# Performance work log

Measured on AMD Instinct MI355X. Metric: run time of the kernel, lower is better.

## Reference

```python
import jax, jax.numpy as jnp
import numpy as np

EPS = 1e-10  # PyTorch Adagrad epsilon convention: denom = sqrt(m) + eps


def setup_inputs() -> dict:
    key = jax.random.key(0)
    k1, k2, k3, k4 = jax.random.split(key, 4)
    N, V, D = 262144, 500000, 64
    return {
        "gradients": jax.random.normal(k1, (N, D), dtype=jnp.float32),
        "weights": jax.random.normal(k2, (V, D), dtype=jnp.float32),
        "moments": jax.random.uniform(k3, (V, D), dtype=jnp.float32),
        "indices": jax.random.randint(k4, (N,), 0, V, dtype=jnp.int64),
        "learning_rate": jnp.ones((), dtype=jnp.float32),
        "valid_count": 200000,  # python int (static)
    }


def reference(gradients, weights, moments, indices, learning_rate, valid_count):
    # Sparse Adagrad: gather rows by index, m += g^2, w -= lr*g/(sqrt(m)+eps), scatter back.
    N = gradients.shape[0]
    valid = (jnp.arange(N) < valid_count)[:, None]          # [N,1] mask of valid rows
    g = jnp.where(valid, gradients, jnp.zeros((), gradients.dtype))  # [N,D]

    # Accumulate squared grads into moments (duplicate indices accumulate).
    moments_new = moments.at[indices].add(g * g)            # [V,D]

    # Per-row denominator uses the fully-accumulated moment of that index.
    denom = jnp.sqrt(moments_new[indices]) + EPS            # [N,D] gather
    weights_new = weights.at[indices].add(-learning_rate * g / denom)  # [V,D]

    return weights_new, moments_new
```

## Files before the change

### kernel.cpp

```cpp
#include <hip/hip_runtime.h>

#define ADAGRAD_EPS 1e-10f

typedef float f4 __attribute__((ext_vector_type(4)));


__global__ void build_lists_kernel(const int* __restrict__ idx,
                                   const int* __restrict__ vc_p,
                                   int* __restrict__ head,
                                   int* __restrict__ next) {
    int vc = *vc_p;
    int r = blockIdx.x * blockDim.x + threadIdx.x;
    if (r >= vc) return;
    int i = idx[r];
    next[r] = atomicExch(&head[i], r);
}

__global__ __launch_bounds__(256) void apply_kernel(
        const f4* __restrict__ g4,
        const f4* __restrict__ w4,
        const f4* __restrict__ m4,
        const int* __restrict__ head,
        const int* __restrict__ next,
        const float* __restrict__ lr_p,
        f4* __restrict__ ow4,
        f4* __restrict__ om4,
        int V) {
    int t = blockIdx.x * blockDim.x + threadIdx.x;
    int v = t >> 3;
    if (v >= V) return;
    int d2 = (t & 7) << 1;
    int off = v * 16 + d2;

    int r = head[v];
    f4 w0 = w4[off];
    f4 w1 = w4[off + 1];
    f4 m0 = m4[off];
    f4 m1 = m4[off + 1];

    if (r < 0) {
        __builtin_nontemporal_store(w0, ow4 + off);
        __builtin_nontemporal_store(w1, ow4 + off + 1);
        __builtin_nontemporal_store(m0, om4 + off);
        __builtin_nontemporal_store(m1, om4 + off + 1);
        return;
    }

    float lr = *lr_p;

    f4 s10 = {0.f, 0.f, 0.f, 0.f};
    f4 s11 = s10, s20 = s10, s21 = s10;
    while (r >= 0) {
        int go = r * 16 + d2;
        f4 g0 = g4[go];
        f4 g1 = g4[go + 1];
        r = next[r];
        s10 += g0; s20 += g0 * g0;
        s11 += g1; s21 += g1 * g1;
    }

    f4 mn0 = m0 + s20;
    f4 mn1 = m1 + s21;
    __builtin_nontemporal_store(mn0, om4 + off);
    __builtin_nontemporal_store(mn1, om4 + off + 1);

    f4 wn0, wn1;
    wn0.x = w0.x - lr * s10.x / (sqrtf(mn0.x) + ADAGRAD_EPS);
    wn0.y = w0.y - lr * s10.y / (sqrtf(mn0.y) + ADAGRAD_EPS);
    wn0.z = w0.z - lr * s10.z / (sqrtf(mn0.z) + ADAGRAD_EPS);
    wn0.w = w0.w - lr * s10.w / (sqrtf(mn0.w) + ADAGRAD_EPS);
    wn1.x = w1.x - lr * s11.x / (sqrtf(mn1.x) + ADAGRAD_EPS);
    wn1.y = w1.y - lr * s11.y / (sqrtf(mn1.y) + ADAGRAD_EPS);
    wn1.z = w1.z - lr * s11.z / (sqrtf(mn1.z) + ADAGRAD_EPS);
    wn1.w = w1.w - lr * s11.w / (sqrtf(mn1.w) + ADAGRAD_EPS);
    __builtin_nontemporal_store(wn0, ow4 + off);
    __builtin_nontemporal_store(wn1, ow4 + off + 1);
}

extern "C" void kernel_launch(void* const* d_in, const int* in_sizes, int n_in,
                              void* d_out, int out_size, void* d_ws, size_t ws_size,
                              hipStream_t stream) {
    const float* g   = (const float*)d_in[0];
    const float* w   = (const float*)d_in[1];
    const float* m   = (const float*)d_in[2];
    const int*   idx = (const int*)d_in[3];
    const float* lr  = (const float*)d_in[4];
    const int*   vc  = (const int*)d_in[5];

    long long ND = in_sizes[0];
    long long VD = in_sizes[1];
    int N = (int)(ND / 64);
    int V = (int)(VD / 64);

    float* out_w = (float*)d_out;
    float* out_m = (float*)d_out + VD;

    int* head = (int*)d_ws;
    int* next = head + V;

    hipMemsetAsync(head, 0xFF, (size_t)V * sizeof(int), stream);

    build_lists_kernel<<<(N + 255) / 256, 256, 0, stream>>>(idx, vc, head, next);

    long long apply_threads = (long long)V * 8;
    apply_kernel<<<(int)((apply_threads + 255) / 256), 256, 0, stream>>>(
        (const f4*)g, (const f4*)w, (const f4*)m,
        head, next, lr, (f4*)out_w, (f4*)out_m, V);
}
```

Measured before the change: 486.0 us.

## Split apply into dense copy and compacted update over touched rows

```diff
diff --git a/kernel.cpp b/kernel.cpp
--- a/kernel.cpp
+++ b/kernel.cpp
@@ -8,27 +8,48 @@
 __global__ void build_lists_kernel(const int* __restrict__ idx,
                                    const int* __restrict__ vc_p,
                                    int* __restrict__ head,
-                                   int* __restrict__ next) {
+                                   int* __restrict__ next,
+                                   int* __restrict__ tlist,
+                                   int* __restrict__ cnt) {
     int vc = *vc_p;
     int r = blockIdx.x * blockDim.x + threadIdx.x;
     if (r >= vc) return;
     int i = idx[r];
-    next[r] = atomicExch(&head[i], r);
+    int prev = atomicExch(&head[i], r);
+    next[r] = prev;
+    if (prev < 0) {
+        int slot = atomicAdd(cnt, 1);
+        tlist[slot] = i;
+    }
 }
 
-__global__ __launch_bounds__(256) void apply_kernel(
+__global__ __launch_bounds__(256) void copy_kernel(
+        const f4* __restrict__ w4,
+        const f4* __restrict__ m4,
+        f4* __restrict__ ow4,
+        f4* __restrict__ om4,
+        int n4) {
+    int i = blockIdx.x * blockDim.x + threadIdx.x;
+    if (i >= n4) return;
+    ow4[i] = w4[i];
+    om4[i] = m4[i];
+}
+
+__global__ __launch_bounds__(256) void update_kernel(
         const f4* __restrict__ g4,
         const f4* __restrict__ w4,
         const f4* __restrict__ m4,
         const int* __restrict__ head,
         const int* __restrict__ next,
+        const int* __restrict__ tlist,
+        const int* __restrict__ cnt,
         const float* __restrict__ lr_p,
         f4* __restrict__ ow4,
-        f4* __restrict__ om4,
-        int V) {
+        f4* __restrict__ om4) {
     int t = blockIdx.x * blockDim.x + threadIdx.x;
-    int v = t >> 3;
-    if (v >= V) return;
+    int s = t >> 3;
+    if (s >= *cnt) return;
+    int v = tlist[s];
     int d2 = (t & 7) << 1;
     int off = v * 16 + d2;
 
@@ -37,15 +58,6 @@
     f4 w1 = w4[off + 1];
     f4 m0 = m4[off];
     f4 m1 = m4[off + 1];
-
-    if (r < 0) {
-        __builtin_nontemporal_store(w0, ow4 + off);
-        __builtin_nontemporal_store(w1, ow4 + off + 1);
-        __builtin_nontemporal_store(m0, om4 + off);
-        __builtin_nontemporal_store(m1, om4 + off + 1);
-        return;
-    }
-
     float lr = *lr_p;
 
     f4 s10 = {0.f, 0.f, 0.f, 0.f};
@@ -61,8 +73,8 @@
 
     f4 mn0 = m0 + s20;
     f4 mn1 = m1 + s21;
-    __builtin_nontemporal_store(mn0, om4 + off);
-    __builtin_nontemporal_store(mn1, om4 + off + 1);
+    om4[off]     = mn0;
+    om4[off + 1] = mn1;
 
     f4 wn0, wn1;
     wn0.x = w0.x - lr * s10.x / (sqrtf(mn0.x) + ADAGRAD_EPS);
@@ -73,8 +85,8 @@
     wn1.y = w1.y - lr * s11.y / (sqrtf(mn1.y) + ADAGRAD_EPS);
     wn1.z = w1.z - lr * s11.z / (sqrtf(mn1.z) + ADAGRAD_EPS);
     wn1.w = w1.w - lr * s11.w / (sqrtf(mn1.w) + ADAGRAD_EPS);
-    __builtin_nontemporal_store(wn0, ow4 + off);
-    __builtin_nontemporal_store(wn1, ow4 + off + 1);
+    ow4[off]     = wn0;
+    ow4[off + 1] = wn1;
 }
 
 extern "C" void kernel_launch(void* const* d_in, const int* in_sizes, int n_in,
@@ -95,15 +107,23 @@
     float* out_w = (float*)d_out;
     float* out_m = (float*)d_out + VD;
 
-    int* head = (int*)d_ws;
-    int* next = head + V;
+    int* head  = (int*)d_ws;
+    int* next  = head + V;
+    int* tlist = next + N;
+    int* cnt   = tlist + N;
 
     hipMemsetAsync(head, 0xFF, (size_t)V * sizeof(int), stream);
+    hipMemsetAsync(cnt, 0, sizeof(int), stream);
 
-    build_lists_kernel<<<(N + 255) / 256, 256, 0, stream>>>(idx, vc, head, next);
+    build_lists_kernel<<<(N + 255) / 256, 256, 0, stream>>>(
+        idx, vc, head, next, tlist, cnt);
 
-    long long apply_threads = (long long)V * 8;
-    apply_kernel<<<(int)((apply_threads + 255) / 256), 256, 0, stream>>>(
+    int n4 = (int)(VD / 4);
+    copy_kernel<<<(n4 + 255) / 256, 256, 0, stream>>>(
+        (const f4*)w, (const f4*)m, (f4*)out_w, (f4*)out_m, n4);
+
+    long long upd_threads = (long long)N * 8;
+    update_kernel<<<(int)((upd_threads + 255) / 256), 256, 0, stream>>>(
         (const f4*)g, (const f4*)w, (const f4*)m,
-        head, next, lr, (f4*)out_w, (f4*)out_m, V);
+        head, next, tlist, cnt, lr, (f4*)out_w, (f4*)out_m);
 }
```

Result: slower. 536.3 us (+10.4%).

## Interleave two row chains per thread with one f4 per lane

Applied to the files above, without the earlier changes.

```diff
diff --git a/kernel.cpp b/kernel.cpp
--- a/kernel.cpp
+++ b/kernel.cpp
@@ -25,56 +25,69 @@
         const float* __restrict__ lr_p,
         f4* __restrict__ ow4,
         f4* __restrict__ om4,
-        int V) {
+        int V, int H) {
     int t = blockIdx.x * blockDim.x + threadIdx.x;
-    int v = t >> 3;
-    if (v >= V) return;
-    int d2 = (t & 7) << 1;
-    int off = v * 16 + d2;
+    int v0 = t >> 4;
+    if (v0 >= H) return;
+    int d = t & 15;
+    int v1 = v0 + H;
+    bool has1 = (v1 < V);
 
-    int r = head[v];
-    f4 w0 = w4[off];
-    f4 w1 = w4[off + 1];
-    f4 m0 = m4[off];
-    f4 m1 = m4[off + 1];
+    int off0 = v0 * 16 + d;
+    int off1 = v1 * 16 + d;
 
-    if (r < 0) {
-        __builtin_nontemporal_store(w0, ow4 + off);
-        __builtin_nontemporal_store(w1, ow4 + off + 1);
-        __builtin_nontemporal_store(m0, om4 + off);
-        __builtin_nontemporal_store(m1, om4 + off + 1);
+    int r0 = head[v0];
+    int r1 = has1 ? head[v1] : -1;
+
+    f4 z = {0.f, 0.f, 0.f, 0.f};
+    f4 w0 = w4[off0];
+    f4 m0 = m4[off0];
+    f4 w1 = has1 ? w4[off1] : z;
+    f4 m1 = has1 ? m4[off1] : z;
+
+    float lr = *lr_p;
+
+    if ((r0 & r1) < 0) {
+        ow4[off0] = w0;
+        om4[off0] = m0;
+        if (has1) { ow4[off1] = w1; om4[off1] = m1; }
         return;
     }
 
-    float lr = *lr_p;
-
-    f4 s10 = {0.f, 0.f, 0.f, 0.f};
-    f4 s11 = s10, s20 = s10, s21 = s10;
-    while (r >= 0) {
-        int go = r * 16 + d2;
-        f4 g0 = g4[go];
-        f4 g1 = g4[go + 1];
-        r = next[r];
-        s10 += g0; s20 += g0 * g0;
-        s11 += g1; s21 += g1 * g1;
+    f4 a1 = z, a2 = z;
+    f4 b1 = z, b2 = z;
+    while (r0 >= 0 || r1 >= 0) {
+        if (r0 >= 0) {
+            f4 g0 = g4[r0 * 16 + d];
+            r0 = next[r0];
+            a1 += g0; a2 += g0 * g0;
+        }
+        if (r1 >= 0) {
+            f4 g1 = g4[r1 * 16 + d];
+            r1 = next[r1];
+            b1 += g1; b2 += g1 * g1;
+        }
     }
 
-    f4 mn0 = m0 + s20;
-    f4 mn1 = m1 + s21;
-    __builtin_nontemporal_store(mn0, om4 + off);
-    __builtin_nontemporal_store(mn1, om4 + off + 1);
+    f4 mn0 = m0 + a2;
+    om4[off0] = mn0;
+    f4 wn0;
+    wn0.x = w0.x - lr * a1.x / (sqrtf(mn0.x) + ADAGRAD_EPS);
+    wn0.y = w0.y - lr * a1.y / (sqrtf(mn0.y) + ADAGRAD_EPS);
+    wn0.z = w0.z - lr * a1.z / (sqrtf(mn0.z) + ADAGRAD_EPS);
+    wn0.w = w0.w - lr * a1.w / (sqrtf(mn0.w) + ADAGRAD_EPS);
+    ow4[off0] = wn0;
 
-    f4 wn0, wn1;
-    wn0.x = w0.x - lr * s10.x / (sqrtf(mn0.x) + ADAGRAD_EPS);
-    wn0.y = w0.y - lr * s10.y / (sqrtf(mn0.y) + ADAGRAD_EPS);
-    wn0.z = w0.z - lr * s10.z / (sqrtf(mn0.z) + ADAGRAD_EPS);
-    wn0.w = w0.w - lr * s10.w / (sqrtf(mn0.w) + ADAGRAD_EPS);
-    wn1.x = w1.x - lr * s11.x / (sqrtf(mn1.x) + ADAGRAD_EPS);
-    wn1.y = w1.y - lr * s11.y / (sqrtf(mn1.y) + ADAGRAD_EPS);
-    wn1.z = w1.z - lr * s11.z / (sqrtf(mn1.z) + ADAGRAD_EPS);
-    wn1.w = w1.w - lr * s11.w / (sqrtf(mn1.w) + ADAGRAD_EPS);
-    __builtin_nontemporal_store(wn0, ow4 + off);
-    __builtin_nontemporal_store(wn1, ow4 + off + 1);
+    if (has1) {
+        f4 mn1 = m1 + b2;
+        om4[off1] = mn1;
+        f4 wn1;
+        wn1.x = w1.x - lr * b1.x / (sqrtf(mn1.x) + ADAGRAD_EPS);
+        wn1.y = w1.y - lr * b1.y / (sqrtf(mn1.y) + ADAGRAD_EPS);
+        wn1.z = w1.z - lr * b1.z / (sqrtf(mn1.z) + ADAGRAD_EPS);
+        wn1.w = w1.w - lr * b1.w / (sqrtf(mn1.w) + ADAGRAD_EPS);
+        ow4[off1] = wn1;
+    }
 }
 
 extern "C" void kernel_launch(void* const* d_in, const int* in_sizes, int n_in,
@@ -102,8 +115,9 @@
 
     build_lists_kernel<<<(N + 255) / 256, 256, 0, stream>>>(idx, vc, head, next);
 
-    long long apply_threads = (long long)V * 8;
+    int H = (V + 1) / 2;
+    long long apply_threads = (long long)H * 16;
     apply_kernel<<<(int)((apply_threads + 255) / 256), 256, 0, stream>>>(
         (const f4*)g, (const f4*)w, (const f4*)m,
-        head, next, lr, (f4*)out_w, (f4*)out_m, V);
+        head, next, lr, (f4*)out_w, (f4*)out_m, V, H);
 }
```

New measurement: 465.3 us. 4.2% less time.
